# Kernel tuning notes

Hardware: AMD Instinct MI355X
Metric: run time of the kernel (lower is better)

The kernel has to match this reference:

```python
import jax, jax.numpy as jnp
import numpy as np

B, N, DIM = 4, 2048, 512
H, HD = 8, 64  # n_heads, head_dim; inner_dim = H*HD = 512
SCALE = 1.0 / float(np.sqrt(HD))

def setup_inputs() -> dict:
    key = jax.random.key(0)
    k1, k2, k3 = jax.random.split(key, 3)
    x = jax.random.normal(k1, (B, N, DIM), dtype=jnp.float32)
    w_qkv = jax.random.normal(k2, (DIM, 3 * H * HD), dtype=jnp.float32) * 0.02
    w_out = jax.random.normal(k3, (H * HD, DIM), dtype=jnp.float32) * 0.02
    b_out = jnp.zeros((DIM,), dtype=jnp.float32)
    return {"x": x, "w_qkv": w_qkv, "w_out": w_out, "b_out": b_out}

def reference(x, w_qkv, w_out, b_out):
    b, n, c = x.shape
    qkv = x @ w_qkv                                   # [B,N,3*H*HD]
    qkv = qkv.reshape(b, n, 3, H, HD)
    q = qkv[:, :, 0].transpose(0, 2, 1, 3)            # [B,H,N,HD]
    k = qkv[:, :, 1].transpose(0, 2, 1, 3)
    v = qkv[:, :, 2].transpose(0, 2, 1, 3)
    # non-softmax attention: (Q K^T) V scaled by 1/sqrt(d) and 1/N
    attn = jnp.einsum('bhnd,bhmd->bhnm', q, k) * (SCALE / n)  # [B,H,N,N]
    out = jnp.einsum('bhnm,bhmd->bhnd', attn, v)               # [B,H,N,HD]
    out = out.transpose(0, 2, 1, 3).reshape(b, n, H * HD)
    return out @ w_out + b_out
```

## Files before the change

### kernel.cpp

```cpp
#include <hip/hip_runtime.h>
#include <stdint.h>

typedef unsigned short u16;
typedef __attribute__((ext_vector_type(8))) __bf16 bf16x8;
typedef __attribute__((ext_vector_type(8))) unsigned short u16x8;
typedef __attribute__((ext_vector_type(4))) float f32x4;

#define AS1 __attribute__((address_space(1)))
#define AS3 __attribute__((address_space(3)))

__device__ __forceinline__ u16 f2bf(float f) {
  uint32_t u = __builtin_bit_cast(uint32_t, f);
  u += 0x7FFFu + ((u >> 16) & 1u);
  return (u16)(u >> 16);
}
__device__ __forceinline__ float bf2f(u16 h) {
  uint32_t u = ((uint32_t)h) << 16;
  return __builtin_bit_cast(float, u);
}
__device__ __forceinline__ void gload16(const void* g, void* l) {
  __builtin_amdgcn_global_load_lds((AS1 void*)g, (AS3 void*)l, 16, 0, 0);
}

__global__ __launch_bounds__(256) void prep(const float4* __restrict__ x,
                                            ushort4* __restrict__ x_bf,
                                            const float* __restrict__ w,
                                            u16* __restrict__ wt) {
  __shared__ u16 tile[32][33];
  const int bid = blockIdx.x;
  if (bid < 4096) {
    int i = bid * 256 + threadIdx.x;
    float4 v = x[i];
    ushort4 o;
    o.x = f2bf(v.x); o.y = f2bf(v.y); o.z = f2bf(v.z); o.w = f2bf(v.w);
    x_bf[i] = o;
  } else {
    int tb = bid - 4096;
    int c0 = (tb % 48) * 32, r0 = (tb / 48) * 32;
    int tx = threadIdx.x & 31, ty = threadIdx.x >> 5;
    #pragma unroll
    for (int rr = ty; rr < 32; rr += 8)
      tile[rr][tx] = f2bf(w[(size_t)(r0 + rr) * 1536 + c0 + tx]);
    __syncthreads();
    #pragma unroll
    for (int rr = ty; rr < 32; rr += 8)
      wt[(size_t)(c0 + rr) * 512 + r0 + tx] = tile[tx][rr];
  }
}

template<bool OUT_F32, bool BIAS, int NFRAG>
__global__ __launch_bounds__(256) void gemm_bt64(
    const u16* __restrict__ A, int lda, long long strideA,
    const u16* __restrict__ Bt, int ldb, long long strideB,
    void* __restrict__ C, int ldc, long long strideC,
    const float* __restrict__ bias, int K)
{
  constexpr int BN = NFRAG * 32;
  const int nwgx = gridDim.x, nwgy = gridDim.y;
  const int nwg = nwgx * nwgy * gridDim.z;
  const int hw = blockIdx.x + nwgx * (blockIdx.y + nwgy * blockIdx.z);
  const int cpx = nwg >> 3;
  const int swz = (hw & 7) * cpx + (hw >> 3);
  const int bx = swz % nwgx;
  const int tmp = swz / nwgx;
  const int by = tmp % nwgy;
  const int bz = tmp / nwgy;

  const int bcol = bx * BN;
  const int brow = by * 128;
  const u16* Ab = A + (size_t)bz * strideA;
  const u16* Bb = Bt + (size_t)bz * strideB;

  __shared__ u16 Asm[128 * 64];
  __shared__ u16 Bsm[BN * 64];

  const int tid = threadIdx.x;
  const int wid = tid >> 6;
  const int lane = tid & 63;
  const int fr = lane & 15, fq = lane >> 4;
  const int wr = wid >> 1, wc = wid & 1;
  const int srow = lane >> 3;
  const int scol = ((lane & 7) ^ srow) * 8;
  const int xr = (fr & 7) * 8;

  f32x4 acc[4][NFRAG];
  #pragma unroll
  for (int m = 0; m < 4; ++m)
    #pragma unroll
    for (int n = 0; n < NFRAG; ++n)
      acc[m][n] = (f32x4)0.0f;

  for (int kt = 0; kt < K; kt += 64) {
    #pragma unroll
    for (int q = 0; q < 4; ++q) {
      int seg = wid * 4 + q;
      int row = seg * 8 + srow;
      gload16(Ab + (size_t)(brow + row) * lda + kt + scol, &Asm[seg * 512]);
    }
    #pragma unroll
    for (int q = 0; q < NFRAG; ++q) {
      int seg = wid * NFRAG + q;
      int row = seg * 8 + srow;
      gload16(Bb + (size_t)(bcol + row) * ldb + kt + scol, &Bsm[seg * 512]);
    }
    __syncthreads();

    #pragma unroll
    for (int kk = 0; kk < 2; ++kk) {
      bf16x8 af[4], bg[NFRAG];
      #pragma unroll
      for (int m = 0; m < 4; ++m)
        af[m] = *(const bf16x8*)&Asm[(wr * 64 + m * 16 + fr) * 64 + ((kk * 32 + fq * 8) ^ xr)];
      #pragma unroll
      for (int n = 0; n < NFRAG; ++n)
        bg[n] = *(const bf16x8*)&Bsm[(wc * (NFRAG * 16) + n * 16 + fr) * 64 + ((kk * 32 + fq * 8) ^ xr)];
      #pragma unroll
      for (int m = 0; m < 4; ++m)
        #pragma unroll
        for (int n = 0; n < NFRAG; ++n)
          acc[m][n] = __builtin_amdgcn_mfma_f32_16x16x32_bf16(af[m], bg[n], acc[m][n], 0, 0, 0);
    }
    __syncthreads();
  }

  #pragma unroll
  for (int m = 0; m < 4; ++m) {
    #pragma unroll
    for (int n = 0; n < NFRAG; ++n) {
      #pragma unroll
      for (int j = 0; j < 4; ++j) {
        int row = brow + wr * 64 + m * 16 + fq * 4 + j;
        int col = bcol + wc * (NFRAG * 16) + n * 16 + fr;
        float v = acc[m][n][j];
        if constexpr (OUT_F32) {
          if constexpr (BIAS) v += bias[col];
          ((float*)C)[(size_t)bz * strideC + (size_t)row * ldc + col] = v;
        } else {
          ((u16*)C)[(size_t)bz * strideC + (size_t)row * ldc + col] = f2bf(v);
        }
      }
    }
  }
}

#define KTV_SPLIT 16
__device__ __forceinline__ void ktv_load(const u16* __restrict__ base, int n0, int h, int t,
                                         u16x8& a, u16x8& b) {
  int row0 = t >> 4, part0 = t & 15;
  int col0 = (part0 < 8) ? (512 + h * 64 + part0 * 8) : (1024 + h * 64 + (part0 - 8) * 8);
  a = *(const u16x8*)(base + (size_t)(n0 + row0) * 1536 + col0);
  int idx1 = 256 + t;
  int row1 = idx1 >> 4, part1 = idx1 & 15;
  int col1 = (part1 < 8) ? (512 + h * 64 + part1 * 8) : (1024 + h * 64 + (part1 - 8) * 8);
  b = *(const u16x8*)(base + (size_t)(n0 + row1) * 1536 + col1);
}

__global__ __launch_bounds__(256) void ktv_partial(const u16* __restrict__ qkv,
                                                   float* __restrict__ Mpart) {
  const int s = blockIdx.x;
  const int bh = blockIdx.y;
  const int b = bh >> 3, h = bh & 7;
  const int t = threadIdx.x;
  __shared__ float smem[4096];
  float* Kf = smem;
  float* Vf = smem + 2048;

  const int nsub = t >> 6;
  const int slot = t & 63;
  const int d0 = (slot >> 2) * 4;
  const int e0 = (slot & 3) * 16;

  float acc[4][16];
  #pragma unroll
  for (int i = 0; i < 4; ++i)
    #pragma unroll
    for (int j = 0; j < 16; ++j) acc[i][j] = 0.f;

  const u16* base = qkv + (size_t)b * 2048 * 1536;
  const int row0 = t >> 4, part0 = t & 15;
  const int idx1 = 256 + t, row1 = idx1 >> 4, part1 = idx1 & 15;
  float* dst0 = (part0 < 8) ? &Kf[row0 * 64 + part0 * 8] : &Vf[row0 * 64 + (part0 - 8) * 8];
  float* dst1 = (part1 < 8) ? &Kf[row1 * 64 + part1 * 8] : &Vf[row1 * 64 + (part1 - 8) * 8];

  u16x8 cur0, cur1, nxt0, nxt1;
  ktv_load(base, s * 128, h, t, cur0, cur1);

  for (int c = 0; c < 4; ++c) {
    __syncthreads();
    #pragma unroll
    for (int j = 0; j < 8; ++j) dst0[j] = bf2f(cur0[j]);
    #pragma unroll
    for (int j = 0; j < 8; ++j) dst1[j] = bf2f(cur1[j]);
    if (c < 3) ktv_load(base, s * 128 + (c + 1) * 32, h, t, nxt0, nxt1);
    __syncthreads();
    #pragma unroll
    for (int nn = 0; nn < 8; ++nn) {
      int n = nsub * 8 + nn;
      f32x4 kq = *(const f32x4*)&Kf[n * 64 + d0];
      f32x4 v0 = *(const f32x4*)&Vf[n * 64 + e0];
      f32x4 v1 = *(const f32x4*)&Vf[n * 64 + e0 + 4];
      f32x4 v2 = *(const f32x4*)&Vf[n * 64 + e0 + 8];
      f32x4 v3 = *(const f32x4*)&Vf[n * 64 + e0 + 12];
      #pragma unroll
      for (int i = 0; i < 4; ++i) {
        float ki = kq[i];
        #pragma unroll
        for (int j = 0; j < 4; ++j) {
          acc[i][j]      += ki * v0[j];
          acc[i][4 + j]  += ki * v1[j];
          acc[i][8 + j]  += ki * v2[j];
          acc[i][12 + j] += ki * v3[j];
        }
      }
    }
    cur0 = nxt0; cur1 = nxt1;
  }

  __syncthreads();
  float* Msm = smem;
  #pragma unroll
  for (int p = 0; p < 4; ++p) {
    if (nsub == p) {
      #pragma unroll
      for (int i = 0; i < 4; ++i)
        #pragma unroll
        for (int j = 0; j < 16; ++j) {
          float* q = &Msm[(d0 + i) * 64 + e0 + j];
          *q = (p == 0) ? acc[i][j] : (*q + acc[i][j]);
        }
    }
    __syncthreads();
  }
  float4* d4 = (float4*)(Mpart + ((size_t)bh * KTV_SPLIT + s) * 4096);
  const float4* s4 = (const float4*)smem;
  #pragma unroll
  for (int r = 0; r < 4; ++r) d4[t + r * 256] = s4[t + r * 256];
}

__global__ __launch_bounds__(256) void reduce_m(const float* __restrict__ Mpart,
                                                float* __restrict__ M, float scale) {
  int i = blockIdx.x * 256 + threadIdx.x;
  int bh = i >> 12;
  int off = i & 4095;
  const float* src = Mpart + ((size_t)bh * KTV_SPLIT) * 4096 + off;
  float s = 0.f;
  #pragma unroll
  for (int p = 0; p < KTV_SPLIT; ++p) s += src[(size_t)p * 4096];
  M[i] = s * scale;
}

__global__ __launch_bounds__(256) void make_pt2(const float* __restrict__ M,
                                                const float* __restrict__ w_out,
                                                u16* __restrict__ Pt) {
  const int ct = blockIdx.x;
  const int bh = blockIdx.y;
  const int b = bh >> 3, h = bh & 7;
  const int t = threadIdx.x;
  __shared__ float Msm[64 * 64];
  {
    const float4* src = (const float4*)(M + (size_t)bh * 4096);
    float4* dst = (float4*)Msm;
    #pragma unroll
    for (int r = 0; r < 4; ++r) dst[t + r * 256] = src[t + r * 256];
  }
  __syncthreads();
  const int c = ct * 64 + (t & 63);
  const int d0 = (t >> 6) * 16;
  float acc[16];
  #pragma unroll
  for (int j = 0; j < 16; ++j) acc[j] = 0.f;
  const float* wcol = w_out + (size_t)h * 64 * 512 + c;
  #pragma unroll 4
  for (int e = 0; e < 64; ++e) {
    float w = wcol[(size_t)e * 512];
    #pragma unroll
    for (int j = 0; j < 16; ++j)
      acc[j] += Msm[(d0 + j) * 64 + e] * w;
  }
  ushort4 ov[4];
  #pragma unroll
  for (int r = 0; r < 4; ++r) {
    ov[r].x = f2bf(acc[r * 4 + 0]);
    ov[r].y = f2bf(acc[r * 4 + 1]);
    ov[r].z = f2bf(acc[r * 4 + 2]);
    ov[r].w = f2bf(acc[r * 4 + 3]);
  }
  ushort4* dst = (ushort4*)(Pt + (size_t)b * 262144 + (size_t)c * 512 + h * 64 + d0);
  #pragma unroll
  for (int r = 0; r < 4; ++r) dst[r] = ov[r];
}

extern "C" void kernel_launch(void* const* d_in, const int* in_sizes, int n_in,
                              void* d_out, int out_size, void* d_ws, size_t ws_size,
                              hipStream_t stream) {
  const float* x     = (const float*)d_in[0];
  const float* w_qkv = (const float*)d_in[1];
  const float* w_out = (const float*)d_in[2];
  const float* b_out = (const float*)d_in[3];
  float* out = (float*)d_out;
  char* ws = (char*)d_ws;
  const long long MB = 1ll << 20;

  u16*   x_bf   = (u16*)(ws);
  u16*   wqkv_t = (u16*)(ws + 8 * MB);
  u16*   qkv    = (u16*)(ws + 10 * MB);
  float* Mpart  = (float*)(ws + 34 * MB);
  float* M      = (float*)(ws);
  u16*   Pt     = (u16*)(ws + 42 * MB);

  prep<<<dim3(4096 + 768), dim3(256), 0, stream>>>(
      (const float4*)x, (ushort4*)x_bf, w_qkv, wqkv_t);
  gemm_bt64<false, false, 4><<<dim3(12, 64, 1), dim3(256), 0, stream>>>(
      x_bf, 512, 0ll, wqkv_t, 512, 0ll, qkv, 1536, 0ll, nullptr, 512);
  ktv_partial<<<dim3(KTV_SPLIT, 32), dim3(256), 0, stream>>>(qkv, Mpart);
  reduce_m<<<dim3(512), dim3(256), 0, stream>>>(Mpart, M, 0.125f / 2048.0f);
  make_pt2<<<dim3(8, 32), dim3(256), 0, stream>>>(M, w_out, Pt);
  gemm_bt64<true, true, 2><<<dim3(8, 16, 4), dim3(256), 0, stream>>>(
      qkv, 1536, 2048ll * 1536, Pt, 512, 262144ll, out, 512, 2048ll * 512, b_out, 512);
}
```

Measured before the change: 63.85 us.

## Fuse KtV, reduce and projection kernels with grid barriers; stage GEMM epilogue via LDS

```diff
diff --git a/kernel.cpp b/kernel.cpp
--- a/kernel.cpp
+++ b/kernel.cpp
@@ -22,13 +22,28 @@
   __builtin_amdgcn_global_load_lds((AS1 void*)g, (AS3 void*)l, 16, 0, 0);
 }
 
+__device__ __forceinline__ void gridbar(unsigned* ctr, unsigned target) {
+  __syncthreads();
+  if (threadIdx.x == 0) {
+    __threadfence();
+    atomicAdd(ctr, 1u);
+    while (__hip_atomic_load(ctr, __ATOMIC_ACQUIRE, __HIP_MEMORY_SCOPE_AGENT) < target) {
+      __builtin_amdgcn_s_sleep(1);
+    }
+    __threadfence();
+  }
+  __syncthreads();
+}
+
 __global__ __launch_bounds__(256) void prep(const float4* __restrict__ x,
                                             ushort4* __restrict__ x_bf,
                                             const float* __restrict__ w,
-                                            u16* __restrict__ wt) {
+                                            u16* __restrict__ wt,
+                                            unsigned* __restrict__ bar) {
   __shared__ u16 tile[32][33];
   const int bid = blockIdx.x;
   if (bid < 4096) {
+    if (bid == 0 && threadIdx.x < 16) bar[threadIdx.x] = 0;
     int i = bid * 256 + threadIdx.x;
     float4 v = x[i];
     ushort4 o;
@@ -71,8 +86,9 @@
   const u16* Ab = A + (size_t)bz * strideA;
   const u16* Bb = Bt + (size_t)bz * strideB;
 
-  __shared__ u16 Asm[128 * 64];
-  __shared__ u16 Bsm[BN * 64];
+  __shared__ alignas(16) u16 SMEM[17408];
+  u16* Asm = SMEM;
+  u16* Bsm = SMEM + 128 * 64;
 
   const int tid = threadIdx.x;
   const int wid = tid >> 6;
@@ -123,22 +139,54 @@
     __syncthreads();
   }
 
-  #pragma unroll
-  for (int m = 0; m < 4; ++m) {
-    #pragma unroll
-    for (int n = 0; n < NFRAG; ++n) {
-      #pragma unroll
-      for (int j = 0; j < 4; ++j) {
-        int row = brow + wr * 64 + m * 16 + fq * 4 + j;
-        int col = bcol + wc * (NFRAG * 16) + n * 16 + fr;
-        float v = acc[m][n][j];
-        if constexpr (OUT_F32) {
-          if constexpr (BIAS) v += bias[col];
-          ((float*)C)[(size_t)bz * strideC + (size_t)row * ldc + col] = v;
-        } else {
-          ((u16*)C)[(size_t)bz * strideC + (size_t)row * ldc + col] = f2bf(v);
+  if constexpr (OUT_F32) {
+    constexpr int PAD = BN + 4;
+    float* Osm = (float*)SMEM;
+    #pragma unroll
+    for (int m = 0; m < 4; ++m)
+      #pragma unroll
+      for (int n = 0; n < NFRAG; ++n)
+        #pragma unroll
+        for (int j = 0; j < 4; ++j) {
+          int row = wr * 64 + m * 16 + fq * 4 + j;
+          int col = wc * (NFRAG * 16) + n * 16 + fr;
+          Osm[row * PAD + col] = acc[m][n][j];
         }
+    __syncthreads();
+    float* Cb = (float*)C + (size_t)bz * strideC;
+    constexpr int C4 = BN / 4;
+    #pragma unroll
+    for (int r = 0; r < 128 * C4 / 256; ++r) {
+      int flat = tid + r * 256;
+      int row = flat / C4, c4 = (flat % C4) * 4;
+      float4 v = *(const float4*)&Osm[row * PAD + c4];
+      if constexpr (BIAS) {
+        float4 bb = *(const float4*)&bias[bcol + c4];
+        v.x += bb.x; v.y += bb.y; v.z += bb.z; v.w += bb.w;
       }
+      *(float4*)&Cb[(size_t)(brow + row) * ldc + bcol + c4] = v;
+    }
+  } else {
+    constexpr int PADu = BN + 8;
+    u16* Osm = (u16*)SMEM;
+    #pragma unroll
+    for (int m = 0; m < 4; ++m)
+      #pragma unroll
+      for (int n = 0; n < NFRAG; ++n)
+        #pragma unroll
+        for (int j = 0; j < 4; ++j) {
+          int row = wr * 64 + m * 16 + fq * 4 + j;
+          int col = wc * (NFRAG * 16) + n * 16 + fr;
+          Osm[row * PADu + col] = f2bf(acc[m][n][j]);
+        }
+    __syncthreads();
+    u16* Cb = (u16*)C + (size_t)bz * strideC;
+    constexpr int C8 = BN / 8;
+    #pragma unroll
+    for (int r = 0; r < 128 * C8 / 256; ++r) {
+      int flat = tid + r * 256;
+      int row = flat / C8, c8 = (flat % C8) * 8;
+      *(u16x8*)&Cb[(size_t)(brow + row) * ldc + bcol + c8] = *(const u16x8*)&Osm[row * PADu + c8];
     }
   }
 }
@@ -155,139 +203,144 @@
   b = *(const u16x8*)(base + (size_t)(n0 + row1) * 1536 + col1);
 }
 
-__global__ __launch_bounds__(256) void ktv_partial(const u16* __restrict__ qkv,
-                                                   float* __restrict__ Mpart) {
+__global__ __launch_bounds__(256) void ktv_all(const u16* __restrict__ qkv,
+                                               float* __restrict__ Mpart,
+                                               float* __restrict__ M,
+                                               const float* __restrict__ w_out,
+                                               u16* __restrict__ Pt,
+                                               unsigned* __restrict__ bar,
+                                               float scale) {
   const int s = blockIdx.x;
   const int bh = blockIdx.y;
+  const int flat = bh * 16 + s;
   const int b = bh >> 3, h = bh & 7;
   const int t = threadIdx.x;
   __shared__ float smem[4096];
   float* Kf = smem;
   float* Vf = smem + 2048;
 
-  const int nsub = t >> 6;
-  const int slot = t & 63;
-  const int d0 = (slot >> 2) * 4;
-  const int e0 = (slot & 3) * 16;
-
-  float acc[4][16];
-  #pragma unroll
-  for (int i = 0; i < 4; ++i)
-    #pragma unroll
-    for (int j = 0; j < 16; ++j) acc[i][j] = 0.f;
-
-  const u16* base = qkv + (size_t)b * 2048 * 1536;
-  const int row0 = t >> 4, part0 = t & 15;
-  const int idx1 = 256 + t, row1 = idx1 >> 4, part1 = idx1 & 15;
-  float* dst0 = (part0 < 8) ? &Kf[row0 * 64 + part0 * 8] : &Vf[row0 * 64 + (part0 - 8) * 8];
-  float* dst1 = (part1 < 8) ? &Kf[row1 * 64 + part1 * 8] : &Vf[row1 * 64 + (part1 - 8) * 8];
-
-  u16x8 cur0, cur1, nxt0, nxt1;
-  ktv_load(base, s * 128, h, t, cur0, cur1);
-
-  for (int c = 0; c < 4; ++c) {
-    __syncthreads();
-    #pragma unroll
-    for (int j = 0; j < 8; ++j) dst0[j] = bf2f(cur0[j]);
-    #pragma unroll
-    for (int j = 0; j < 8; ++j) dst1[j] = bf2f(cur1[j]);
-    if (c < 3) ktv_load(base, s * 128 + (c + 1) * 32, h, t, nxt0, nxt1);
-    __syncthreads();
-    #pragma unroll
-    for (int nn = 0; nn < 8; ++nn) {
-      int n = nsub * 8 + nn;
-      f32x4 kq = *(const f32x4*)&Kf[n * 64 + d0];
-      f32x4 v0 = *(const f32x4*)&Vf[n * 64 + e0];
-      f32x4 v1 = *(const f32x4*)&Vf[n * 64 + e0 + 4];
-      f32x4 v2 = *(const f32x4*)&Vf[n * 64 + e0 + 8];
-      f32x4 v3 = *(const f32x4*)&Vf[n * 64 + e0 + 12];
-      #pragma unroll
-      for (int i = 0; i < 4; ++i) {
-        float ki = kq[i];
-        #pragma unroll
-        for (int j = 0; j < 4; ++j) {
-          acc[i][j]      += ki * v0[j];
-          acc[i][4 + j]  += ki * v1[j];
-          acc[i][8 + j]  += ki * v2[j];
-          acc[i][12 + j] += ki * v3[j];
+  {
+    const int nsub = t >> 6;
+    const int slot = t & 63;
+    const int d0 = (slot >> 2) * 4;
+    const int e0 = (slot & 3) * 16;
+
+    float acc[4][16];
+    #pragma unroll
+    for (int i = 0; i < 4; ++i)
+      #pragma unroll
+      for (int j = 0; j < 16; ++j) acc[i][j] = 0.f;
+
+    const u16* base = qkv + (size_t)b * 2048 * 1536;
+    const int row0 = t >> 4, part0 = t & 15;
+    const int idx1 = 256 + t, row1 = idx1 >> 4, part1 = idx1 & 15;
+    float* dst0 = (part0 < 8) ? &Kf[row0 * 64 + part0 * 8] : &Vf[row0 * 64 + (part0 - 8) * 8];
+    float* dst1 = (part1 < 8) ? &Kf[row1 * 64 + part1 * 8] : &Vf[row1 * 64 + (part1 - 8) * 8];
+
+    u16x8 cur0, cur1, nxt0, nxt1;
+    ktv_load(base, s * 128, h, t, cur0, cur1);
+
+    for (int c = 0; c < 4; ++c) {
+      __syncthreads();
+      #pragma unroll
+      for (int j = 0; j < 8; ++j) dst0[j] = bf2f(cur0[j]);
+      #pragma unroll
+      for (int j = 0; j < 8; ++j) dst1[j] = bf2f(cur1[j]);
+      if (c < 3) ktv_load(base, s * 128 + (c + 1) * 32, h, t, nxt0, nxt1);
+      __syncthreads();
+      #pragma unroll
+      for (int nn = 0; nn < 8; ++nn) {
+        int n = nsub * 8 + nn;
+        f32x4 kq = *(const f32x4*)&Kf[n * 64 + d0];
+        f32x4 v0 = *(const f32x4*)&Vf[n * 64 + e0];
+        f32x4 v1 = *(const f32x4*)&Vf[n * 64 + e0 + 4];
+        f32x4 v2 = *(const f32x4*)&Vf[n * 64 + e0 + 8];
+        f32x4 v3 = *(const f32x4*)&Vf[n * 64 + e0 + 12];
+        #pragma unroll
+        for (int i = 0; i < 4; ++i) {
+          float ki = kq[i];
+          #pragma unroll
+          for (int j = 0; j < 4; ++j) {
+            acc[i][j]      += ki * v0[j];
+            acc[i][4 + j]  += ki * v1[j];
+            acc[i][8 + j]  += ki * v2[j];
+            acc[i][12 + j] += ki * v3[j];
+          }
         }
       }
-    }
-    cur0 = nxt0; cur1 = nxt1;
-  }
-
-  __syncthreads();
-  float* Msm = smem;
-  #pragma unroll
-  for (int p = 0; p < 4; ++p) {
-    if (nsub == p) {
-      #pragma unroll
-      for (int i = 0; i < 4; ++i)
-        #pragma unroll
-        for (int j = 0; j < 16; ++j) {
-          float* q = &Msm[(d0 + i) * 64 + e0 + j];
-          *q = (p == 0) ? acc[i][j] : (*q + acc[i][j]);
-        }
-    }
-    __syncthreads();
-  }
-  float4* d4 = (float4*)(Mpart + ((size_t)bh * KTV_SPLIT + s) * 4096);
-  const float4* s4 = (const float4*)smem;
-  #pragma unroll
-  for (int r = 0; r < 4; ++r) d4[t + r * 256] = s4[t + r * 256];
-}
-
-__global__ __launch_bounds__(256) void reduce_m(const float* __restrict__ Mpart,
-                                                float* __restrict__ M, float scale) {
-  int i = blockIdx.x * 256 + threadIdx.x;
-  int bh = i >> 12;
-  int off = i & 4095;
-  const float* src = Mpart + ((size_t)bh * KTV_SPLIT) * 4096 + off;
-  float s = 0.f;
-  #pragma unroll
-  for (int p = 0; p < KTV_SPLIT; ++p) s += src[(size_t)p * 4096];
-  M[i] = s * scale;
-}
-
-__global__ __launch_bounds__(256) void make_pt2(const float* __restrict__ M,
-                                                const float* __restrict__ w_out,
-                                                u16* __restrict__ Pt) {
-  const int ct = blockIdx.x;
-  const int bh = blockIdx.y;
-  const int b = bh >> 3, h = bh & 7;
-  const int t = threadIdx.x;
-  __shared__ float Msm[64 * 64];
+      cur0 = nxt0; cur1 = nxt1;
+    }
+
+    __syncthreads();
+    #pragma unroll
+    for (int p = 0; p < 4; ++p) {
+      if (nsub == p) {
+        #pragma unroll
+        for (int i = 0; i < 4; ++i)
+          #pragma unroll
+          for (int j = 0; j < 16; ++j) {
+            float* q = &smem[(d0 + i) * 64 + e0 + j];
+            *q = (p == 0) ? acc[i][j] : (*q + acc[i][j]);
+          }
+      }
+      __syncthreads();
+    }
+    float4* d4 = (float4*)(Mpart + ((size_t)bh * KTV_SPLIT + s) * 4096);
+    const float4* s4 = (const float4*)smem;
+    #pragma unroll
+    for (int r = 0; r < 4; ++r) d4[t + r * 256] = s4[t + r * 256];
+  }
+
+  gridbar(&bar[0], 512);
+
   {
-    const float4* src = (const float4*)(M + (size_t)bh * 4096);
-    float4* dst = (float4*)Msm;
-    #pragma unroll
-    for (int r = 0; r < 4; ++r) dst[t + r * 256] = src[t + r * 256];
-  }
-  __syncthreads();
-  const int c = ct * 64 + (t & 63);
-  const int d0 = (t >> 6) * 16;
-  float acc[16];
-  #pragma unroll
-  for (int j = 0; j < 16; ++j) acc[j] = 0.f;
-  const float* wcol = w_out + (size_t)h * 64 * 512 + c;
-  #pragma unroll 4
-  for (int e = 0; e < 64; ++e) {
-    float w = wcol[(size_t)e * 512];
-    #pragma unroll
-    for (int j = 0; j < 16; ++j)
-      acc[j] += Msm[(d0 + j) * 64 + e] * w;
-  }
-  ushort4 ov[4];
-  #pragma unroll
-  for (int r = 0; r < 4; ++r) {
-    ov[r].x = f2bf(acc[r * 4 + 0]);
-    ov[r].y = f2bf(acc[r * 4 + 1]);
-    ov[r].z = f2bf(acc[r * 4 + 2]);
-    ov[r].w = f2bf(acc[r * 4 + 3]);
-  }
-  ushort4* dst = (ushort4*)(Pt + (size_t)b * 262144 + (size_t)c * 512 + h * 64 + d0);
-  #pragma unroll
-  for (int r = 0; r < 4; ++r) dst[r] = ov[r];
+    int i = flat * 256 + t;
+    int bh2 = i >> 12, off = i & 4095;
+    const float* src = Mpart + ((size_t)bh2 * KTV_SPLIT) * 4096 + off;
+    float ssum = 0.f;
+    #pragma unroll
+    for (int p = 0; p < KTV_SPLIT; ++p) ssum += src[(size_t)p * 4096];
+    M[i] = ssum * scale;
+  }
+
+  gridbar(&bar[1], 512);
+
+  if (flat < 256) {
+    const int ct = flat & 7;
+    const int bh3 = flat >> 3;
+    const int b3 = bh3 >> 3, h3 = bh3 & 7;
+    {
+      const float4* src = (const float4*)(M + (size_t)bh3 * 4096);
+      float4* dst = (float4*)smem;
+      #pragma unroll
+      for (int r = 0; r < 4; ++r) dst[t + r * 256] = src[t + r * 256];
+    }
+    __syncthreads();
+    const int c = ct * 64 + (t & 63);
+    const int d0 = (t >> 6) * 16;
+    float acc[16];
+    #pragma unroll
+    for (int j = 0; j < 16; ++j) acc[j] = 0.f;
+    const float* wcol = w_out + (size_t)h3 * 64 * 512 + c;
+    #pragma unroll 4
+    for (int e = 0; e < 64; ++e) {
+      float w = wcol[(size_t)e * 512];
+      #pragma unroll
+      for (int j = 0; j < 16; ++j)
+        acc[j] += smem[(d0 + j) * 64 + e] * w;
+    }
+    ushort4 ov[4];
+    #pragma unroll
+    for (int r = 0; r < 4; ++r) {
+      ov[r].x = f2bf(acc[r * 4 + 0]);
+      ov[r].y = f2bf(acc[r * 4 + 1]);
+      ov[r].z = f2bf(acc[r * 4 + 2]);
+      ov[r].w = f2bf(acc[r * 4 + 3]);
+    }
+    ushort4* dst = (ushort4*)(Pt + (size_t)b3 * 262144 + (size_t)c * 512 + h3 * 64 + d0);
+    #pragma unroll
+    for (int r = 0; r < 4; ++r) dst[r] = ov[r];
+  }
 }
 
 extern "C" void kernel_launch(void* const* d_in, const int* in_sizes, int n_in,
@@ -301,20 +354,20 @@
   char* ws = (char*)d_ws;
   const long long MB = 1ll << 20;
 
-  u16*   x_bf   = (u16*)(ws);
-  u16*   wqkv_t = (u16*)(ws + 8 * MB);
-  u16*   qkv    = (u16*)(ws + 10 * MB);
-  float* Mpart  = (float*)(ws + 34 * MB);
-  float* M      = (float*)(ws);
-  u16*   Pt     = (u16*)(ws + 42 * MB);
+  u16*      x_bf   = (u16*)(ws);
+  u16*      wqkv_t = (u16*)(ws + 8 * MB);
+  u16*      qkv    = (u16*)(ws + 10 * MB);
+  float*    Mpart  = (float*)(ws + 34 * MB);
+  float*    M      = (float*)(ws);
+  u16*      Pt     = (u16*)(ws + 42 * MB);
+  unsigned* bar    = (unsigned*)(ws + 46 * MB);
 
   prep<<<dim3(4096 + 768), dim3(256), 0, stream>>>(
-      (const float4*)x, (ushort4*)x_bf, w_qkv, wqkv_t);
+      (const float4*)x, (ushort4*)x_bf, w_qkv, wqkv_t, bar);
   gemm_bt64<false, false, 4><<<dim3(12, 64, 1), dim3(256), 0, stream>>>(
       x_bf, 512, 0ll, wqkv_t, 512, 0ll, qkv, 1536, 0ll, nullptr, 512);
-  ktv_partial<<<dim3(KTV_SPLIT, 32), dim3(256), 0, stream>>>(qkv, Mpart);
-  reduce_m<<<dim3(512), dim3(256), 0, stream>>>(Mpart, M, 0.125f / 2048.0f);
-  make_pt2<<<dim3(8, 32), dim3(256), 0, stream>>>(M, w_out, Pt);
+  ktv_all<<<dim3(KTV_SPLIT, 32), dim3(256), 0, stream>>>(
+      qkv, Mpart, M, w_out, Pt, bar, 0.125f / 2048.0f);
   gemm_bt64<true, true, 2><<<dim3(8, 16, 4), dim3(256), 0, stream>>>(
       qkv, 1536, 2048ll * 1536, Pt, 512, 262144ll, out, 512, 2048ll * 512, b_out, 512);
 }
```

New measurement: 194.1 us. 3.04x slower.

## Compute K^T V partials with bf16 MFMA instead of scalar FP32 FMAs

Applied to the files above, without the earlier changes.

```diff
diff --git a/kernel.cpp b/kernel.cpp
--- a/kernel.cpp
+++ b/kernel.cpp
@@ -144,95 +144,82 @@
 }
 
 #define KTV_SPLIT 16
-__device__ __forceinline__ void ktv_load(const u16* __restrict__ base, int n0, int h, int t,
-                                         u16x8& a, u16x8& b) {
-  int row0 = t >> 4, part0 = t & 15;
-  int col0 = (part0 < 8) ? (512 + h * 64 + part0 * 8) : (1024 + h * 64 + (part0 - 8) * 8);
-  a = *(const u16x8*)(base + (size_t)(n0 + row0) * 1536 + col0);
-  int idx1 = 256 + t;
-  int row1 = idx1 >> 4, part1 = idx1 & 15;
-  int col1 = (part1 < 8) ? (512 + h * 64 + part1 * 8) : (1024 + h * 64 + (part1 - 8) * 8);
-  b = *(const u16x8*)(base + (size_t)(n0 + row1) * 1536 + col1);
-}
-
 __global__ __launch_bounds__(256) void ktv_partial(const u16* __restrict__ qkv,
                                                    float* __restrict__ Mpart) {
   const int s = blockIdx.x;
   const int bh = blockIdx.y;
   const int b = bh >> 3, h = bh & 7;
   const int t = threadIdx.x;
-  __shared__ float smem[4096];
-  float* Kf = smem;
-  float* Vf = smem + 2048;
-
-  const int nsub = t >> 6;
-  const int slot = t & 63;
-  const int d0 = (slot >> 2) * 4;
-  const int e0 = (slot & 3) * 16;
-
-  float acc[4][16];
-  #pragma unroll
-  for (int i = 0; i < 4; ++i)
-    #pragma unroll
-    for (int j = 0; j < 16; ++j) acc[i][j] = 0.f;
-
-  const u16* base = qkv + (size_t)b * 2048 * 1536;
-  const int row0 = t >> 4, part0 = t & 15;
-  const int idx1 = 256 + t, row1 = idx1 >> 4, part1 = idx1 & 15;
-  float* dst0 = (part0 < 8) ? &Kf[row0 * 64 + part0 * 8] : &Vf[row0 * 64 + (part0 - 8) * 8];
-  float* dst1 = (part1 < 8) ? &Kf[row1 * 64 + part1 * 8] : &Vf[row1 * 64 + (part1 - 8) * 8];
-
-  u16x8 cur0, cur1, nxt0, nxt1;
-  ktv_load(base, s * 128, h, t, cur0, cur1);
-
-  for (int c = 0; c < 4; ++c) {
+  __shared__ alignas(16) u16 SM[2 * 64 * 136];
+  u16* Kt = SM;
+  u16* Vt = SM + 64 * 136;
+  float* Msm = (float*)SM;
+
+  const u16* base = qkv + (size_t)b * 2048 * 1536 + (size_t)(s * 128) * 1536;
+  u16x8 v[8];
+  #pragma unroll
+  for (int it = 0; it < 8; ++it) {
+    int c = it * 256 + t;
+    int n = c >> 4, part = c & 15;
+    int col = (part < 8) ? (512 + h * 64 + part * 8) : (1024 + h * 64 + (part - 8) * 8);
+    v[it] = *(const u16x8*)(base + (size_t)n * 1536 + col);
+  }
+  #pragma unroll
+  for (int it = 0; it < 8; ++it) {
+    int c = it * 256 + t;
+    int n = c >> 4, part = c & 15;
+    int p8 = part & 7;
+    u16* mat = (part < 8) ? Kt : Vt;
+    int ncol = n ^ (p8 << 3);
+    #pragma unroll
+    for (int j = 0; j < 8; ++j)
+      mat[(p8 * 8 + j) * 136 + ncol] = v[it][j];
+  }
+  __syncthreads();
+
+  const int wid = t >> 6, lane = t & 63;
+  const int fr = lane & 15, fq = lane >> 4;
+  const int kbase = wid * 32 + fq * 8;
+  f32x4 acc[4][4];
+  #pragma unroll
+  for (int m = 0; m < 4; ++m)
+    #pragma unroll
+    for (int n = 0; n < 4; ++n) acc[m][n] = (f32x4)0.0f;
+  bf16x8 af[4], bg[4];
+  #pragma unroll
+  for (int m = 0; m < 4; ++m) {
+    int d = m * 16 + fr;
+    af[m] = *(const bf16x8*)&Kt[d * 136 + (kbase ^ ((d >> 3) << 3))];
+  }
+  #pragma unroll
+  for (int n = 0; n < 4; ++n) {
+    int e = n * 16 + fr;
+    bg[n] = *(const bf16x8*)&Vt[e * 136 + (kbase ^ ((e >> 3) << 3))];
+  }
+  #pragma unroll
+  for (int m = 0; m < 4; ++m)
+    #pragma unroll
+    for (int n = 0; n < 4; ++n)
+      acc[m][n] = __builtin_amdgcn_mfma_f32_16x16x32_bf16(af[m], bg[n], acc[m][n], 0, 0, 0);
+  __syncthreads();
+
+  #pragma unroll
+  for (int p = 0; p < 4; ++p) {
+    if (wid == p) {
+      #pragma unroll
+      for (int m = 0; m < 4; ++m)
+        #pragma unroll
+        for (int n = 0; n < 4; ++n)
+          #pragma unroll
+          for (int j = 0; j < 4; ++j) {
+            float* q = &Msm[(m * 16 + fq * 4 + j) * 64 + n * 16 + fr];
+            *q = (p == 0) ? acc[m][n][j] : (*q + acc[m][n][j]);
+          }
+    }
     __syncthreads();
-    #pragma unroll
-    for (int j = 0; j < 8; ++j) dst0[j] = bf2f(cur0[j]);
-    #pragma unroll
-    for (int j = 0; j < 8; ++j) dst1[j] = bf2f(cur1[j]);
-    if (c < 3) ktv_load(base, s * 128 + (c + 1) * 32, h, t, nxt0, nxt1);
-    __syncthreads();
-    #pragma unroll
-    for (int nn = 0; nn < 8; ++nn) {
-      int n = nsub * 8 + nn;
-      f32x4 kq = *(const f32x4*)&Kf[n * 64 + d0];
-      f32x4 v0 = *(const f32x4*)&Vf[n * 64 + e0];
-      f32x4 v1 = *(const f32x4*)&Vf[n * 64 + e0 + 4];
-      f32x4 v2 = *(const f32x4*)&Vf[n * 64 + e0 + 8];
-      f32x4 v3 = *(const f32x4*)&Vf[n * 64 + e0 + 12];
-      #pragma unroll
-      for (int i = 0; i < 4; ++i) {
-        float ki = kq[i];
-        #pragma unroll
-        for (int j = 0; j < 4; ++j) {
-          acc[i][j]      += ki * v0[j];
-          acc[i][4 + j]  += ki * v1[j];
-          acc[i][8 + j]  += ki * v2[j];
-          acc[i][12 + j] += ki * v3[j];
-        }
-      }
-    }
-    cur0 = nxt0; cur1 = nxt1;
-  }
-
-  __syncthreads();
-  float* Msm = smem;
-  #pragma unroll
-  for (int p = 0; p < 4; ++p) {
-    if (nsub == p) {
-      #pragma unroll
-      for (int i = 0; i < 4; ++i)
-        #pragma unroll
-        for (int j = 0; j < 16; ++j) {
-          float* q = &Msm[(d0 + i) * 64 + e0 + j];
-          *q = (p == 0) ? acc[i][j] : (*q + acc[i][j]);
-        }
-    }
-    __syncthreads();
   }
   float4* d4 = (float4*)(Mpart + ((size_t)bh * KTV_SPLIT + s) * 4096);
-  const float4* s4 = (const float4*)smem;
+  const float4* s4 = (const float4*)Msm;
   #pragma unroll
   for (int r = 0; r < 4; ++r) d4[t + r * 256] = s4[t + r * 256];
 }
```

Result: faster. 61.50 us (-3.7%).
